# Kernel tuning notes

Hardware: AMD Instinct MI355X
Metric: run time of the kernel (lower is better)

The kernel has to match this reference:

```python
import jax, jax.numpy as jnp
import numpy as np
from jax import lax

V, E, H, K = 100000, 256, 512, 12
B, T = 64, 256
START, END, PAD = 10, 11, 0
NEG = -100000.0


def setup_inputs() -> dict:
    key = jax.random.key(0)
    ks = jax.random.split(key, 16)
    Hd = H // 2
    def n(k, shape, s=0.1):
        return jax.random.normal(k, shape, jnp.float32) * s
    sentence = jax.random.randint(ks[0], (B, T), 0, V)
    sentence_chars = jnp.zeros((B, T, 16), jnp.int32)
    emb = jax.random.normal(ks[1], (V, E), jnp.float32)
    Wih_f, Whh_f = n(ks[2], (4 * Hd, E)), n(ks[3], (4 * Hd, Hd))
    bih_f, bhh_f = n(ks[4], (4 * Hd,)), n(ks[5], (4 * Hd,))
    Wih_b, Whh_b = n(ks[6], (4 * Hd, E)), n(ks[7], (4 * Hd, Hd))
    bih_b, bhh_b = n(ks[8], (4 * Hd,)), n(ks[9], (4 * Hd,))
    Wp, bp = n(ks[10], (K, H)), n(ks[11], (K,))
    # transitions[i, j] = score of transitioning from tag j to tag i
    trans = jax.random.normal(ks[12], (K, K), jnp.float32)
    trans = trans.at[START, :].set(NEG)
    trans = trans.at[:, END].set(NEG)
    trans = trans.at[:, PAD].set(NEG)
    trans = trans.at[PAD, :].set(NEG)
    trans = trans.at[PAD, PAD].set(0.0)
    trans = trans.at[PAD, END].set(0.0)
    h0 = jax.random.normal(ks[13], (2, B, Hd), jnp.float32)
    c0 = jax.random.normal(ks[14], (2, B, Hd), jnp.float32)
    return dict(sentence=sentence, sentence_chars=sentence_chars, emb=emb,
                Wih_f=Wih_f, Whh_f=Whh_f, bih_f=bih_f, bhh_f=bhh_f,
                Wih_b=Wih_b, Whh_b=Whh_b, bih_b=bih_b, bhh_b=bhh_b,
                Wp=Wp, bp=bp, transitions=trans, h0=h0, c0=c0)


def _lstm_dir(x, Wih, Whh, bih, bhh, h, c, reverse):
    # x: [B, T, E] -> hs: [B, T, Hd]; PyTorch LSTM gate order i,f,g,o
    def step(carry, xt):
        h, c = carry
        g = xt @ Wih.T + bih + h @ Whh.T + bhh
        i, f, gg, o = jnp.split(g, 4, axis=-1)
        c = jax.nn.sigmoid(f) * c + jax.nn.sigmoid(i) * jnp.tanh(gg)
        h = jax.nn.sigmoid(o) * jnp.tanh(c)
        return (h, c), h
    _, hs = lax.scan(step, (h, c), jnp.swapaxes(x, 0, 1), reverse=reverse)
    return jnp.swapaxes(hs, 0, 1)


def _viterbi(features, transitions, lengths):
    b, t, k = features.shape
    score0 = jnp.full((b, k), -10000.0, features.dtype).at[:, START].set(0.0)
    def step(score, feat_t):
        m = score[:, None, :] + transitions[None]  # [B, K(to), K(from)]
        bptr = jnp.argmax(m, axis=-1)              # [B, K]
        new = jnp.max(m, axis=-1) + feat_t
        return new, bptr
    final, bptrs = lax.scan(step, score0, jnp.swapaxes(features, 0, 1))  # bptrs [T,B,K]
    best_score = jnp.max(final, axis=-1)
    best_tag = jnp.argmax(final, axis=-1)
    ts = jnp.arange(t)
    def backtrack(x, inp):
        tt, bp = inp  # bp: [B, K]
        emit = x      # p_t (valid where tt < length)
        nxt = jnp.take_along_axis(bp, x[:, None], axis=1)[:, 0]
        x = jnp.where(tt < lengths, nxt, x)
        return x, emit
    _, ps = lax.scan(backtrack, best_tag, (ts, bptrs), reverse=True)  # [T, B]
    paths = jnp.swapaxes(ps, 0, 1)
    paths = jnp.where(jnp.arange(t)[None, :] < lengths[:, None], paths, -1)
    return paths, best_score


def reference(sentence, sentence_chars, emb, Wih_f, Whh_f, bih_f, bhh_f,
              Wih_b, Whh_b, bih_b, bhh_b, Wp, bp, transitions, h0, c0):
    mask = sentence > 0
    lengths = mask.sum(axis=1)
    x = emb[sentence]  # [B, T, E]
    hf = _lstm_dir(x, Wih_f, Whh_f, bih_f, bhh_f, h0[0], c0[0], False)
    hb = _lstm_dir(x, Wih_b, Whh_b, bih_b, bhh_b, h0[1], c0[1], True)
    feats = jnp.concatenate([hf, hb], axis=-1) @ Wp.T + bp  # [B, T, K]
    paths, best_score = _viterbi(feats, transitions, lengths)
    return paths, best_score
```

## Files before the change

### kernel.cpp

```cpp
#include <hip/hip_runtime.h>


#define NB 64
#define NT 256
#define NKTAG 12
#define START_TAG 10
#define KK_SLAB 32
#define KK_REG 16
#define KK_STRM 8

typedef unsigned short u16;
typedef _Float16 half2v __attribute__((ext_vector_type(2)));
typedef _Float16 half8 __attribute__((ext_vector_type(8)));
typedef float f32x4 __attribute__((ext_vector_type(4)));

__device__ __forceinline__ float b2f(u16 u) {
  union { unsigned int i; float f; } v; v.i = ((unsigned int)u) << 16; return v.f;
}
__device__ __forceinline__ u16 f2b(float f) {
  union { float f; unsigned int i; } v; v.f = f;
  unsigned int r = v.i + 0x7FFFu + ((v.i >> 16) & 1u);
  return (u16)(r >> 16);
}
__device__ __forceinline__ u16 f2h(float f) {
  union { _Float16 h; u16 u; } v; v.h = (_Float16)f; return v.u;
}
__device__ __forceinline__ unsigned int pkh(float x, float y) {
  return (unsigned int)f2h(x) | ((unsigned int)f2h(y) << 16);
}
__device__ __forceinline__ float fsig(float x) { return 1.0f / (1.0f + __expf(-x)); }
__device__ __forceinline__ float ftanh(float x) { return 2.0f / (1.0f + __expf(-2.0f * x)) - 1.0f; }

__device__ __forceinline__ float dot2h(unsigned int a, unsigned int b, float c) {
#if __has_builtin(__builtin_amdgcn_fdot2)
  union { unsigned int u; half2v h; } va, vb;
  va.u = a; vb.u = b;
  return __builtin_amdgcn_fdot2(va.h, vb.h, c, false);
#else
  float d;
  asm("v_dot2_f32_f16 %0, %1, %2, %3" : "=v"(d) : "v"(a), "v"(b), "v"(c));
  return d;
#endif
}

__global__ __launch_bounds__(256) void pack_whh(const float* __restrict__ Whf,
                                                const float* __restrict__ Whb,
                                                const float* __restrict__ Wp,
                                                uint4* __restrict__ WT,
                                                unsigned int* __restrict__ WpH) {
  if (blockIdx.x == 256) {
    for (int it = 0; it < 12; ++it) {
      int idx = it * 256 + threadIdx.x;
      int k = idx >> 8, cc = idx & 255;
      WpH[idx] = pkh(Wp[(size_t)k * 512 + 2 * cc], Wp[(size_t)k * 512 + 2 * cc + 1]);
    }
    return;
  }
  int gid = blockIdx.x * 256 + threadIdx.x;
  int d = gid >> 15;
  int rem = gid & 32767;
  int kk = rem >> 8, j = rem & 255;
  const float* W = d ? Whb : Whf;
  int k0 = kk * 2;
  uint4 o;
  o.x = pkh(W[(size_t)j * 256 + k0],         W[(size_t)j * 256 + k0 + 1]);
  o.y = pkh(W[(size_t)(j + 256) * 256 + k0], W[(size_t)(j + 256) * 256 + k0 + 1]);
  o.z = pkh(W[(size_t)(j + 512) * 256 + k0], W[(size_t)(j + 512) * 256 + k0 + 1]);
  o.w = pkh(W[(size_t)(j + 768) * 256 + k0], W[(size_t)(j + 768) * 256 + k0 + 1]);
  WT[gid] = o;
}

__global__ __launch_bounds__(256) void gemm_x(const int* __restrict__ sent,
                                              const float* __restrict__ emb,
                                              const float* __restrict__ Wf,
                                              const float* __restrict__ Wb,
                                              const float* __restrict__ bihf,
                                              const float* __restrict__ bhhf,
                                              const float* __restrict__ bihb,
                                              const float* __restrict__ bhhb,
                                              u16* __restrict__ X4) {
  __shared__ _Float16 A_lds[128][40];
  __shared__ _Float16 B_lds[64][40];
  __shared__ int tok[128];
  __shared__ u16 Xs[128][80];
  int tid = threadIdx.x;
  int in = blockIdx.x;
  int im = blockIdx.y;
  int d = in >> 4, j0 = (in & 15) * 16;
  if (tid < 128) tok[tid] = sent[im * 128 + tid];

  int w = tid >> 6, l = tid & 63;
  int lrow = l & 15, lk = l >> 4;
  f32x4 acc[2][4];
#pragma unroll
  for (int mt = 0; mt < 2; ++mt)
#pragma unroll
    for (int nt = 0; nt < 4; ++nt) acc[mt][nt] = (f32x4)0.0f;

  int arow = tid >> 1, akh = tid & 1;
  int brow = tid & 63, bkq = tid >> 6;
  int r_w = ((brow >> 4) << 8) + j0 + (brow & 15);
  const float* wrow = (d ? Wb : Wf) + (size_t)r_w * 256;

  for (int kc = 0; kc < 8; ++kc) {
    int k0 = kc * 32;
    __syncthreads();
    {
      const float* ap = emb + (size_t)tok[arow] * 256 + k0 + akh * 16;
#pragma unroll
      for (int q = 0; q < 2; ++q) {
        float4 v0 = *(const float4*)(ap + q * 8);
        float4 v1 = *(const float4*)(ap + q * 8 + 4);
        uint4 pk;
        pk.x = pkh(v0.x, v0.y); pk.y = pkh(v0.z, v0.w);
        pk.z = pkh(v1.x, v1.y); pk.w = pkh(v1.z, v1.w);
        *(uint4*)&A_lds[arow][akh * 16 + q * 8] = pk;
      }
    }
    {
      float4 v0 = *(const float4*)(wrow + k0 + bkq * 8);
      float4 v1 = *(const float4*)(wrow + k0 + bkq * 8 + 4);
      uint4 pk;
      pk.x = pkh(v0.x, v0.y); pk.y = pkh(v0.z, v0.w);
      pk.z = pkh(v1.x, v1.y); pk.w = pkh(v1.z, v1.w);
      *(uint4*)&B_lds[brow][bkq * 8] = pk;
    }
    __syncthreads();
    half8 af[2], bf[4];
#pragma unroll
    for (int mt = 0; mt < 2; ++mt)
      af[mt] = *(const half8*)&A_lds[w * 32 + mt * 16 + lrow][lk * 8];
#pragma unroll
    for (int nt = 0; nt < 4; ++nt)
      bf[nt] = *(const half8*)&B_lds[nt * 16 + lrow][lk * 8];
#pragma unroll
    for (int mt = 0; mt < 2; ++mt)
#pragma unroll
      for (int nt = 0; nt < 4; ++nt)
        acc[mt][nt] = __builtin_amdgcn_mfma_f32_16x16x32_f16(af[mt], bf[nt], acc[mt][nt], 0, 0, 0);
  }
  float bias[4];
#pragma unroll
  for (int nt = 0; nt < 4; ++nt) {
    int rr = nt * 256 + j0 + lrow;
    bias[nt] = d ? (bihb[rr] + bhhb[rr]) : (bihf[rr] + bhhf[rr]);
  }
  __syncthreads();
#pragma unroll
  for (int mt = 0; mt < 2; ++mt)
#pragma unroll
    for (int r = 0; r < 4; ++r) {
      int row = w * 32 + mt * 16 + lk * 4 + r;
      uint2 pk;
      pk.x = (unsigned int)f2b(acc[mt][0][r] + bias[0]) |
             ((unsigned int)f2b(acc[mt][1][r] + bias[1]) << 16);
      pk.y = (unsigned int)f2b(acc[mt][2][r] + bias[2]) |
             ((unsigned int)f2b(acc[mt][3][r] + bias[3]) << 16);
      *(uint2*)&Xs[row][lrow * 4] = pk;
    }
  __syncthreads();
  int frow = tid >> 1, fh = tid & 1;
  int i = im * 128 + frow;
  int bb = i >> 8, tt = i & 255;
  size_t base = (((size_t)d * NT + tt) * NB + bb) * 1024 + (size_t)j0 * 4 + fh * 32;
#pragma unroll
  for (int q = 0; q < 4; ++q)
    *(uint4*)&X4[base + q * 8] = *(const uint4*)&Xs[frow][fh * 32 + q * 8];
}

__global__ __launch_bounds__(1024, 4) void lstm_scan(const uint4* __restrict__ WT,
                                                     const ushort4* __restrict__ X4,
                                                     const float* __restrict__ h0,
                                                     const float* __restrict__ c0,
                                                     u16* __restrict__ H) {
  int d = blockIdx.x >> 6, b = blockIdx.x & 63;
  int tid = threadIdx.x;
  int jj = tid & 255, g = tid >> 8;
  __shared__ uint4 wlds[KK_SLAB * 256];
  __shared__ uint4 h2s4[32];
  __shared__ float4 plds[3][256];
  const uint4* Ws = WT + (size_t)d * 32768;
  for (int e = tid; e < KK_SLAB * 256; e += 1024) wlds[e] = Ws[e];
  uint4 wreg[KK_REG];
#pragma unroll
  for (int r = 0; r < KK_REG; ++r)
    wreg[r] = Ws[(size_t)(KK_SLAB + g * KK_REG + r) * 256 + jj];
  float c = 0.f;
  if (g == 0) c = c0[((size_t)d * NB + b) * 256 + jj];
  if (tid < 256) ((u16*)h2s4)[tid] = f2h(h0[((size_t)d * NB + b) * 256 + tid]);
  __syncthreads();
  for (int s = 0; s < NT; ++s) {
    int t = d ? (NT - 1 - s) : s;
    ushort4 xg = make_ushort4(0, 0, 0, 0);
    if (g == 0) xg = X4[(((size_t)d * NT + t) * NB + b) * 256 + jj];
    float ai = 0.f, af = 0.f, ag = 0.f, ao = 0.f;
    {
      uint4 hc0 = h2s4[24 + g * 2], hc1 = h2s4[24 + g * 2 + 1];
      unsigned int hp[8] = {hc0.x, hc0.y, hc0.z, hc0.w, hc1.x, hc1.y, hc1.z, hc1.w};
      const uint4* Wp_ = Ws + (size_t)(96 + g * 8) * 256 + jj;
#pragma unroll
      for (int u = 0; u < KK_STRM; ++u) {
        uint4 wv = Wp_[(size_t)u * 256];
        ai = dot2h(wv.x, hp[u], ai); af = dot2h(wv.y, hp[u], af);
        ag = dot2h(wv.z, hp[u], ag); ao = dot2h(wv.w, hp[u], ao);
      }
    }
    {
      uint4 ha0 = h2s4[g * 2], ha1 = h2s4[g * 2 + 1];
      unsigned int hp[8] = {ha0.x, ha0.y, ha0.z, ha0.w, ha1.x, ha1.y, ha1.z, ha1.w};
#pragma unroll
      for (int r = 0; r < 8; ++r) {
        uint4 wv = wlds[((g * 8 + r) << 8) | jj];
        ai = dot2h(wv.x, hp[r], ai); af = dot2h(wv.y, hp[r], af);
        ag = dot2h(wv.z, hp[r], ag); ao = dot2h(wv.w, hp[r], ao);
      }
    }
    {
      uint4 hb0 = h2s4[8 + g * 4], hb1 = h2s4[8 + g * 4 + 1];
      uint4 hb2 = h2s4[8 + g * 4 + 2], hb3 = h2s4[8 + g * 4 + 3];
      unsigned int hp[16] = {hb0.x, hb0.y, hb0.z, hb0.w, hb1.x, hb1.y, hb1.z, hb1.w,
                             hb2.x, hb2.y, hb2.z, hb2.w, hb3.x, hb3.y, hb3.z, hb3.w};
#pragma unroll
      for (int r = 0; r < KK_REG; ++r) {
        uint4 wv = wreg[r];
        ai = dot2h(wv.x, hp[r], ai); af = dot2h(wv.y, hp[r], af);
        ag = dot2h(wv.z, hp[r], ag); ao = dot2h(wv.w, hp[r], ao);
      }
    }
    if (g) plds[g - 1][jj] = make_float4(ai, af, ag, ao);
    __syncthreads();
    if (g == 0) {
      float4 p0 = plds[0][jj], p1 = plds[1][jj], p2 = plds[2][jj];
      ai += p0.x + p1.x + p2.x + b2f(xg.x);
      af += p0.y + p1.y + p2.y + b2f(xg.y);
      ag += p0.z + p1.z + p2.z + b2f(xg.z);
      ao += p0.w + p1.w + p2.w + b2f(xg.w);
      float ii = fsig(ai), ff = fsig(af), gg = ftanh(ag), oo = fsig(ao);
      c = ff * c + ii * gg;
      float h = oo * ftanh(c);
      u16 hu = f2h(h);
      ((u16*)h2s4)[jj] = hu;
      H[(((size_t)d * NB + b) * NT + t) * 256 + jj] = hu;
    }
    __syncthreads();
  }
}

__global__ __launch_bounds__(384) void feats_kernel(const u16* __restrict__ H,
                                                    const unsigned int* __restrict__ WpH,
                                                    const float* __restrict__ bp,
                                                    float* __restrict__ FT) {
  __shared__ uint4 hbuf[32][65];
  __shared__ uint4 wbuf[64][12];
  int tid = threadIdx.x;
  int i0 = blockIdx.x * 32;
  for (int idx = tid; idx < 768; idx += 384) {
    int it = idx / 12, k = idx - it * 12;
    wbuf[it][k] = ((const uint4*)WpH)[k * 64 + it];
  }
  for (int idx = tid; idx < 2048; idx += 384) {
    int row = idx >> 6, c4 = idx & 63;
    int i = i0 + row;
    int b = i >> 8, t = i & 255;
    int dd = c4 >> 5, cc = c4 & 31;
    const uint4* hp = (const uint4*)(H + (((size_t)dd * NB + b) * NT + t) * 256);
    hbuf[row][c4] = hp[cc];
  }
  __syncthreads();
  int row = tid / 12, k = tid - row * 12;
  float s = 0.f;
#pragma unroll 8
  for (int it = 0; it < 64; ++it) {
    uint4 h4 = hbuf[row][it];
    uint4 w4 = wbuf[it][k];
    s = dot2h(h4.x, w4.x, s); s = dot2h(h4.y, w4.y, s);
    s = dot2h(h4.z, w4.z, s); s = dot2h(h4.w, w4.w, s);
  }
  int i = i0 + row;
  FT[(size_t)i * NKTAG + k] = s + bp[k];
}

__global__ __launch_bounds__(64) void viterbi_kernel(const float* __restrict__ FT,
                                                     const float* __restrict__ trans,
                                                     const int* __restrict__ sent,
                                                     float* __restrict__ out) {
  int b = blockIdx.x, tid = threadIdx.x;
  __shared__ float trans_s[12][12];
  __shared__ float s_s[12];
  __shared__ unsigned char bp_s[256][12];
  __shared__ int path_s[256];
  for (int idx = tid; idx < 144; idx += 64) trans_s[idx / 12][idx % 12] = trans[idx];
  int cnt = 0;
#pragma unroll
  for (int q = 0; q < 4; ++q) cnt += (sent[b * NT + q * 64 + tid] > 0) ? 1 : 0;
  for (int off = 32; off; off >>= 1) cnt += __shfl_down(cnt, off);
  int len = __shfl(cnt, 0);
  if (tid < 12) s_s[tid] = (tid == START_TAG) ? 0.f : -10000.f;
  __syncthreads();
  for (int t = 0; t < NT; ++t) {
    float best = 0.f, f = 0.f;
    int barg = 0;
    if (tid < 12) {
      f = FT[((size_t)b * NT + t) * NKTAG + tid];
      best = s_s[0] + trans_s[tid][0];
      barg = 0;
#pragma unroll
      for (int fr = 1; fr < 12; ++fr) {
        float v = s_s[fr] + trans_s[tid][fr];
        if (v > best) { best = v; barg = fr; }
      }
    }
    __syncthreads();
    if (tid < 12) {
      s_s[tid] = best + f;
      bp_s[t][tid] = (unsigned char)barg;
    }
    __syncthreads();
  }
  if (tid == 0) {
    float bs = s_s[0];
    int bt = 0;
    for (int k = 1; k < 12; ++k)
      if (s_s[k] > bs) { bs = s_s[k]; bt = k; }
    out[NB * NT + b] = bs;
    int x = bt;
    for (int tt = NT - 1; tt >= 0; --tt) {
      path_s[tt] = x;
      int nxt = bp_s[tt][x];
      if (tt < len) x = nxt;
    }
  }
  __syncthreads();
#pragma unroll
  for (int q = 0; q < 4; ++q) {
    int t = q * 64 + tid;
    out[b * NT + t] = (t < len) ? (float)path_s[t] : -1.0f;
  }
}

extern "C" void kernel_launch(void* const* d_in, const int* in_sizes, int n_in,
                              void* d_out, int out_size, void* d_ws, size_t ws_size,
                              hipStream_t stream) {
  (void)in_sizes; (void)n_in; (void)out_size; (void)ws_size;
  const int*   sent  = (const int*)d_in[0];
  const float* emb   = (const float*)d_in[2];
  const float* Wih_f = (const float*)d_in[3];
  const float* Whh_f = (const float*)d_in[4];
  const float* bih_f = (const float*)d_in[5];
  const float* bhh_f = (const float*)d_in[6];
  const float* Wih_b = (const float*)d_in[7];
  const float* Whh_b = (const float*)d_in[8];
  const float* bih_b = (const float*)d_in[9];
  const float* bhh_b = (const float*)d_in[10];
  const float* Wp    = (const float*)d_in[11];
  const float* bp    = (const float*)d_in[12];
  const float* trans = (const float*)d_in[13];
  const float* h0    = (const float*)d_in[14];
  const float* c0    = (const float*)d_in[15];
  float* out = (float*)d_out;

  char* w = (char*)d_ws;
  u16*   X4  = (u16*)w;
  uint4* WTH = (uint4*)(w + 67108864);
  float* FT  = (float*)(w + 67108864 + 1048576);
  unsigned int* WpH = (unsigned int*)(w + 68943872);
  u16*   H   = (u16*)(w + 68956160);

  pack_whh<<<dim3(257), dim3(256), 0, stream>>>(Whh_f, Whh_b, Wp, WTH, WpH);
  gemm_x<<<dim3(32, 128), dim3(256), 0, stream>>>(sent, emb, Wih_f, Wih_b,
                                                  bih_f, bhh_f, bih_b, bhh_b, X4);
  lstm_scan<<<dim3(128), dim3(1024), 0, stream>>>(WTH, (const ushort4*)X4, h0, c0, H);
  feats_kernel<<<dim3(512), dim3(384), 0, stream>>>(H, WpH, bp, FT);
  viterbi_kernel<<<dim3(64), dim3(64), 0, stream>>>(FT, trans, sent, out);
}
```

Before: 599.4 us.

## Split each LSTM sequence across two cooperating blocks with flag-synced hidden exchange

The recurrent scan now runs 256 blocks of 512 threads, with each pair of blocks owning half of the hidden units for one (direction, batch) sequence. The partner blocks swap their fp16 hidden halves every timestep through a global slot buffer and spin on per-block step flags. Each thread's recurrent weights now sit entirely in LDS plus 22 registers, so the per-step global streaming of part of Whh goes away. The cost is a cross-block global handshake every timestep, which adds latency, and the scheme needs both blocks of a pair to be co-resident or it can deadlock.

Result: slower. 1.305 ms (+117.8%).

```diff
diff --git a/kernel.cpp b/kernel.cpp
--- a/kernel.cpp
+++ b/kernel.cpp
@@ -5,9 +5,6 @@
 #define NT 256
 #define NKTAG 12
 #define START_TAG 10
-#define KK_SLAB 32
-#define KK_REG 16
-#define KK_STRM 8
 
 typedef unsigned short u16;
 typedef _Float16 half2v __attribute__((ext_vector_type(2)));
@@ -168,64 +165,74 @@
     *(uint4*)&X4[base + q * 8] = *(const uint4*)&Xs[frow][fh * 32 + q * 8];
 }
 
-__global__ __launch_bounds__(1024, 4) void lstm_scan(const uint4* __restrict__ WT,
-                                                     const ushort4* __restrict__ X4,
-                                                     const float* __restrict__ h0,
-                                                     const float* __restrict__ c0,
-                                                     u16* __restrict__ H) {
-  int d = blockIdx.x >> 6, b = blockIdx.x & 63;
+__global__ __launch_bounds__(512, 2) void lstm_scan(const uint4* __restrict__ WT,
+                                                    const ushort4* __restrict__ X4,
+                                                    const float* __restrict__ h0,
+                                                    const float* __restrict__ c0,
+                                                    u16* __restrict__ H,
+                                                    unsigned int* __restrict__ slotb,
+                                                    int* __restrict__ flags) {
+  int bid = blockIdx.x;
+  int d = bid >> 7, b = (bid >> 1) & 63, p = bid & 1;
+  int pbid = bid ^ 1;
   int tid = threadIdx.x;
-  int jj = tid & 255, g = tid >> 8;
-  __shared__ uint4 wlds[KK_SLAB * 256];
+  int jj = tid & 127, g = tid >> 7;
+  int jbase = p << 7;
+  __shared__ uint4 wlds[5120];
   __shared__ uint4 h2s4[32];
-  __shared__ float4 plds[3][256];
+  __shared__ float4 plds[3][128];
   const uint4* Ws = WT + (size_t)d * 32768;
-  for (int e = tid; e < KK_SLAB * 256; e += 1024) wlds[e] = Ws[e];
-  uint4 wreg[KK_REG];
-#pragma unroll
-  for (int r = 0; r < KK_REG; ++r)
-    wreg[r] = Ws[(size_t)(KK_SLAB + g * KK_REG + r) * 256 + jj];
+#pragma unroll
+  for (int r = 0; r < 10; ++r)
+    wlds[((g * 10 + r) << 7) | jj] = Ws[(size_t)(g * 32 + r) * 256 + jbase + jj];
+  uint4 wreg[22];
+#pragma unroll
+  for (int r = 0; r < 22; ++r)
+    wreg[r] = Ws[(size_t)(g * 32 + 10 + r) * 256 + jbase + jj];
   float c = 0.f;
-  if (g == 0) c = c0[((size_t)d * NB + b) * 256 + jj];
+  if (g == 0) c = c0[((size_t)d * NB + b) * 256 + jbase + jj];
   if (tid < 256) ((u16*)h2s4)[tid] = f2h(h0[((size_t)d * NB + b) * 256 + tid]);
   __syncthreads();
   for (int s = 0; s < NT; ++s) {
     int t = d ? (NT - 1 - s) : s;
     ushort4 xg = make_ushort4(0, 0, 0, 0);
-    if (g == 0) xg = X4[(((size_t)d * NT + t) * NB + b) * 256 + jj];
+    if (g == 0) xg = X4[(((size_t)d * NT + t) * NB + b) * 256 + jbase + jj];
+    if (s > 0 && tid < 16) {
+      if (tid == 0) {
+        while (__hip_atomic_load(&flags[pbid], __ATOMIC_RELAXED,
+                                 __HIP_MEMORY_SCOPE_AGENT) < s - 1) {}
+      }
+      asm volatile("" ::: "memory");
+      unsigned pb = (unsigned)(pbid * 2 + ((s - 1) & 1)) * 64 + tid * 4;
+      uint4 hv;
+      hv.x = __hip_atomic_load(&slotb[pb + 0], __ATOMIC_RELAXED, __HIP_MEMORY_SCOPE_AGENT);
+      hv.y = __hip_atomic_load(&slotb[pb + 1], __ATOMIC_RELAXED, __HIP_MEMORY_SCOPE_AGENT);
+      hv.z = __hip_atomic_load(&slotb[pb + 2], __ATOMIC_RELAXED, __HIP_MEMORY_SCOPE_AGENT);
+      hv.w = __hip_atomic_load(&slotb[pb + 3], __ATOMIC_RELAXED, __HIP_MEMORY_SCOPE_AGENT);
+      h2s4[((1 - p) << 4) + tid] = hv;
+    }
+    __syncthreads();
     float ai = 0.f, af = 0.f, ag = 0.f, ao = 0.f;
-    {
-      uint4 hc0 = h2s4[24 + g * 2], hc1 = h2s4[24 + g * 2 + 1];
-      unsigned int hp[8] = {hc0.x, hc0.y, hc0.z, hc0.w, hc1.x, hc1.y, hc1.z, hc1.w};
-      const uint4* Wp_ = Ws + (size_t)(96 + g * 8) * 256 + jj;
-#pragma unroll
-      for (int u = 0; u < KK_STRM; ++u) {
-        uint4 wv = Wp_[(size_t)u * 256];
-        ai = dot2h(wv.x, hp[u], ai); af = dot2h(wv.y, hp[u], af);
-        ag = dot2h(wv.z, hp[u], ag); ao = dot2h(wv.w, hp[u], ao);
-      }
-    }
-    {
-      uint4 ha0 = h2s4[g * 2], ha1 = h2s4[g * 2 + 1];
-      unsigned int hp[8] = {ha0.x, ha0.y, ha0.z, ha0.w, ha1.x, ha1.y, ha1.z, ha1.w};
-#pragma unroll
-      for (int r = 0; r < 8; ++r) {
-        uint4 wv = wlds[((g * 8 + r) << 8) | jj];
-        ai = dot2h(wv.x, hp[r], ai); af = dot2h(wv.y, hp[r], af);
-        ag = dot2h(wv.z, hp[r], ag); ao = dot2h(wv.w, hp[r], ao);
-      }
-    }
-    {
-      uint4 hb0 = h2s4[8 + g * 4], hb1 = h2s4[8 + g * 4 + 1];
-      uint4 hb2 = h2s4[8 + g * 4 + 2], hb3 = h2s4[8 + g * 4 + 3];
-      unsigned int hp[16] = {hb0.x, hb0.y, hb0.z, hb0.w, hb1.x, hb1.y, hb1.z, hb1.w,
-                             hb2.x, hb2.y, hb2.z, hb2.w, hb3.x, hb3.y, hb3.z, hb3.w};
-#pragma unroll
-      for (int r = 0; r < KK_REG; ++r) {
-        uint4 wv = wreg[r];
-        ai = dot2h(wv.x, hp[r], ai); af = dot2h(wv.y, hp[r], af);
-        ag = dot2h(wv.z, hp[r], ag); ao = dot2h(wv.w, hp[r], ao);
-      }
+    uint4 hv[8];
+#pragma unroll
+    for (int q = 0; q < 8; ++q) hv[q] = h2s4[(g << 3) + q];
+    unsigned int hp[32];
+#pragma unroll
+    for (int q = 0; q < 8; ++q) {
+      hp[q * 4 + 0] = hv[q].x; hp[q * 4 + 1] = hv[q].y;
+      hp[q * 4 + 2] = hv[q].z; hp[q * 4 + 3] = hv[q].w;
+    }
+#pragma unroll
+    for (int r = 0; r < 10; ++r) {
+      uint4 wv = wlds[((g * 10 + r) << 7) | jj];
+      ai = dot2h(wv.x, hp[r], ai); af = dot2h(wv.y, hp[r], af);
+      ag = dot2h(wv.z, hp[r], ag); ao = dot2h(wv.w, hp[r], ao);
+    }
+#pragma unroll
+    for (int r = 0; r < 22; ++r) {
+      uint4 wv = wreg[r];
+      ai = dot2h(wv.x, hp[10 + r], ai); af = dot2h(wv.y, hp[10 + r], af);
+      ag = dot2h(wv.z, hp[10 + r], ag); ao = dot2h(wv.w, hp[10 + r], ao);
     }
     if (g) plds[g - 1][jj] = make_float4(ai, af, ag, ao);
     __syncthreads();
@@ -239,10 +246,20 @@
       c = ff * c + ii * gg;
       float h = oo * ftanh(c);
       u16 hu = f2h(h);
-      ((u16*)h2s4)[jj] = hu;
-      H[(((size_t)d * NB + b) * NT + t) * 256 + jj] = hu;
-    }
-    __syncthreads();
+      ((u16*)h2s4)[jbase + jj] = hu;
+      H[(((size_t)d * NB + b) * NT + t) * 256 + jbase + jj] = hu;
+    }
+    __syncthreads();
+    if (tid < 16) {
+      uint4 ho = h2s4[(p << 4) + tid];
+      unsigned ob = (unsigned)(bid * 2 + (s & 1)) * 64 + tid * 4;
+      __hip_atomic_store(&slotb[ob + 0], ho.x, __ATOMIC_RELAXED, __HIP_MEMORY_SCOPE_AGENT);
+      __hip_atomic_store(&slotb[ob + 1], ho.y, __ATOMIC_RELAXED, __HIP_MEMORY_SCOPE_AGENT);
+      __hip_atomic_store(&slotb[ob + 2], ho.z, __ATOMIC_RELAXED, __HIP_MEMORY_SCOPE_AGENT);
+      __hip_atomic_store(&slotb[ob + 3], ho.w, __ATOMIC_RELAXED, __HIP_MEMORY_SCOPE_AGENT);
+    }
+    if (tid == 0)
+      __hip_atomic_store(&flags[bid], s, __ATOMIC_RELEASE, __HIP_MEMORY_SCOPE_AGENT);
   }
 }
 
@@ -263,8 +280,8 @@
     int i = i0 + row;
     int b = i >> 8, t = i & 255;
     int dd = c4 >> 5, cc = c4 & 31;
-    const uint4* hp = (const uint4*)(H + (((size_t)dd * NB + b) * NT + t) * 256);
-    hbuf[row][c4] = hp[cc];
+    const uint4* hpg = (const uint4*)(H + (((size_t)dd * NB + b) * NT + t) * 256);
+    hbuf[row][c4] = hpg[cc];
   }
   __syncthreads();
   int row = tid / 12, k = tid - row * 12;
@@ -362,14 +379,18 @@
   char* w = (char*)d_ws;
   u16*   X4  = (u16*)w;
   uint4* WTH = (uint4*)(w + 67108864);
-  float* FT  = (float*)(w + 67108864 + 1048576);
+  float* FT  = (float*)(w + 68157440);
   unsigned int* WpH = (unsigned int*)(w + 68943872);
   u16*   H   = (u16*)(w + 68956160);
-
+  unsigned int* slotb = (unsigned int*)(w + 85733376);
+  int*   flags = (int*)(w + 85864448);
+
+  hipMemsetAsync(flags, 0xFF, 1024, stream);
   pack_whh<<<dim3(257), dim3(256), 0, stream>>>(Whh_f, Whh_b, Wp, WTH, WpH);
   gemm_x<<<dim3(32, 128), dim3(256), 0, stream>>>(sent, emb, Wih_f, Wih_b,
                                                   bih_f, bhh_f, bih_b, bhh_b, X4);
-  lstm_scan<<<dim3(128), dim3(1024), 0, stream>>>(WTH, (const ushort4*)X4, h0, c0, H);
+  lstm_scan<<<dim3(256), dim3(512), 0, stream>>>(WTH, (const ushort4*)X4, h0, c0,
+                                                 H, slotb, flags);
   feats_kernel<<<dim3(512), dim3(384), 0, stream>>>(H, WpH, bp, FT);
   viterbi_kernel<<<dim3(64), dim3(64), 0, stream>>>(FT, trans, sent, out);
 }
```

## Store LDS-slab and streamed LSTM recurrent weights as FP8

Applied to the files above, without the earlier changes.

The recurrent weights that the LSTM scan keeps in LDS and those it streams from global memory each step are now packed as FP8 by an extra pack block. In the scan they are unpacked to fp32 and combined with an fp32 copy of h kept in shared memory. This halves LDS footprint and the streamed bytes per step, aiming to cut memory traffic on the sequential critical path. In exchange it adds conversion and scalar FMA work in place of packed dot2 instructions, and FP8 weights lose accuracy, which could flip Viterbi paths.

After: 1.847 ms. 208% more time.

```diff
diff --git a/kernel.cpp b/kernel.cpp
--- a/kernel.cpp
+++ b/kernel.cpp
@@ -9,10 +9,20 @@
 #define KK_REG 16
 #define KK_STRM 8
 
+#if defined(__has_builtin)
+#if __has_builtin(__builtin_amdgcn_cvt_pk_f32_fp8) && __has_builtin(__builtin_amdgcn_cvt_pk_fp8_f32)
+#define HAS_FP8 1
+#endif
+#endif
+#ifndef HAS_FP8
+#define HAS_FP8 0
+#endif
+
 typedef unsigned short u16;
 typedef _Float16 half2v __attribute__((ext_vector_type(2)));
 typedef _Float16 half8 __attribute__((ext_vector_type(8)));
 typedef float f32x4 __attribute__((ext_vector_type(4)));
+typedef float f32x2 __attribute__((ext_vector_type(2)));
 
 __device__ __forceinline__ float b2f(u16 u) {
   union { unsigned int i; float f; } v; v.i = ((unsigned int)u) << 16; return v.f;
@@ -47,13 +57,39 @@
                                                 const float* __restrict__ Whb,
                                                 const float* __restrict__ Wp,
                                                 uint4* __restrict__ WT,
-                                                unsigned int* __restrict__ WpH) {
+                                                unsigned int* __restrict__ WpH,
+                                                uint2* __restrict__ WT8) {
   if (blockIdx.x == 256) {
     for (int it = 0; it < 12; ++it) {
       int idx = it * 256 + threadIdx.x;
       int k = idx >> 8, cc = idx & 255;
       WpH[idx] = pkh(Wp[(size_t)k * 512 + 2 * cc], Wp[(size_t)k * 512 + 2 * cc + 1]);
     }
+    return;
+  }
+  if (blockIdx.x == 257) {
+#if HAS_FP8
+    for (int it = 0; it < 128; ++it) {
+      int idx = it * 256 + threadIdx.x;
+      int d = idx >> 14;
+      int rem = idx & 16383;
+      int q = rem >> 8, j = rem & 255;
+      int kk = (q < 32) ? q : (q + 64);
+      const float* W = d ? Whb : Whf;
+      int k0 = kk * 2;
+      int d0 = 0, d1 = 0;
+      d0 = __builtin_amdgcn_cvt_pk_fp8_f32(W[(size_t)j * 256 + k0],
+                                           W[(size_t)(j + 256) * 256 + k0], d0, false);
+      d0 = __builtin_amdgcn_cvt_pk_fp8_f32(W[(size_t)(j + 512) * 256 + k0],
+                                           W[(size_t)(j + 768) * 256 + k0], d0, true);
+      d1 = __builtin_amdgcn_cvt_pk_fp8_f32(W[(size_t)j * 256 + k0 + 1],
+                                           W[(size_t)(j + 256) * 256 + k0 + 1], d1, false);
+      d1 = __builtin_amdgcn_cvt_pk_fp8_f32(W[(size_t)(j + 512) * 256 + k0 + 1],
+                                           W[(size_t)(j + 768) * 256 + k0 + 1], d1, true);
+      uint2 o; o.x = (unsigned int)d0; o.y = (unsigned int)d1;
+      WT8[idx] = o;
+    }
+#endif
     return;
   }
   int gid = blockIdx.x * 256 + threadIdx.x;
@@ -169,6 +205,7 @@
 }
 
 __global__ __launch_bounds__(1024, 4) void lstm_scan(const uint4* __restrict__ WT,
+                                                     const uint2* __restrict__ WT8,
                                                      const ushort4* __restrict__ X4,
                                                      const float* __restrict__ h0,
                                                      const float* __restrict__ c0,
@@ -176,24 +213,81 @@
   int d = blockIdx.x >> 6, b = blockIdx.x & 63;
   int tid = threadIdx.x;
   int jj = tid & 255, g = tid >> 8;
-  __shared__ uint4 wlds[KK_SLAB * 256];
   __shared__ uint4 h2s4[32];
   __shared__ float4 plds[3][256];
+#if HAS_FP8
+  __shared__ uint2 wlds8[KK_SLAB * 256];
+  __shared__ float hf32[256];
+  const uint2* W8 = WT8 + (size_t)d * 16384;
+  for (int e = tid; e < KK_SLAB * 256; e += 1024) wlds8[e] = W8[e];
+#else
+  __shared__ uint4 wlds[KK_SLAB * 256];
+#endif
   const uint4* Ws = WT + (size_t)d * 32768;
+#if !HAS_FP8
   for (int e = tid; e < KK_SLAB * 256; e += 1024) wlds[e] = Ws[e];
+#endif
   uint4 wreg[KK_REG];
 #pragma unroll
   for (int r = 0; r < KK_REG; ++r)
     wreg[r] = Ws[(size_t)(KK_SLAB + g * KK_REG + r) * 256 + jj];
   float c = 0.f;
   if (g == 0) c = c0[((size_t)d * NB + b) * 256 + jj];
-  if (tid < 256) ((u16*)h2s4)[tid] = f2h(h0[((size_t)d * NB + b) * 256 + tid]);
+  if (tid < 256) {
+    float hv = h0[((size_t)d * NB + b) * 256 + tid];
+    ((u16*)h2s4)[tid] = f2h(hv);
+#if HAS_FP8
+    hf32[tid] = hv;
+#endif
+  }
   __syncthreads();
   for (int s = 0; s < NT; ++s) {
     int t = d ? (NT - 1 - s) : s;
     ushort4 xg = make_ushort4(0, 0, 0, 0);
     if (g == 0) xg = X4[(((size_t)d * NT + t) * NB + b) * 256 + jj];
     float ai = 0.f, af = 0.f, ag = 0.f, ao = 0.f;
+#if HAS_FP8
+    const float4* hf4 = (const float4*)hf32;
+    {
+      float4 a0 = hf4[48 + g * 4], a1 = hf4[48 + g * 4 + 1];
+      float4 a2 = hf4[48 + g * 4 + 2], a3 = hf4[48 + g * 4 + 3];
+      float hv[8 * 2] = {a0.x, a0.y, a0.z, a0.w, a1.x, a1.y, a1.z, a1.w,
+                         a2.x, a2.y, a2.z, a2.w, a3.x, a3.y, a3.z, a3.w};
+      const uint2* Wst = W8 + (size_t)(32 + g * 8) * 256 + jj;
+#pragma unroll
+      for (int u = 0; u < KK_STRM; ++u) {
+        uint2 wv = Wst[(size_t)u * 256];
+        f32x2 pif0 = __builtin_amdgcn_cvt_pk_f32_fp8(wv.x, false);
+        f32x2 pgo0 = __builtin_amdgcn_cvt_pk_f32_fp8(wv.x, true);
+        f32x2 pif1 = __builtin_amdgcn_cvt_pk_f32_fp8(wv.y, false);
+        f32x2 pgo1 = __builtin_amdgcn_cvt_pk_f32_fp8(wv.y, true);
+        float hA = hv[2 * u], hB = hv[2 * u + 1];
+        ai += pif0.x * hA + pif1.x * hB;
+        af += pif0.y * hA + pif1.y * hB;
+        ag += pgo0.x * hA + pgo1.x * hB;
+        ao += pgo0.y * hA + pgo1.y * hB;
+      }
+    }
+    {
+      float4 a0 = hf4[g * 4], a1 = hf4[g * 4 + 1];
+      float4 a2 = hf4[g * 4 + 2], a3 = hf4[g * 4 + 3];
+      float hv[8 * 2] = {a0.x, a0.y, a0.z, a0.w, a1.x, a1.y, a1.z, a1.w,
+                         a2.x, a2.y, a2.z, a2.w, a3.x, a3.y, a3.z, a3.w};
+#pragma unroll
+      for (int r = 0; r < 8; ++r) {
+        uint2 wv = wlds8[((g * 8 + r) << 8) | jj];
+        f32x2 pif0 = __builtin_amdgcn_cvt_pk_f32_fp8(wv.x, false);
+        f32x2 pgo0 = __builtin_amdgcn_cvt_pk_f32_fp8(wv.x, true);
+        f32x2 pif1 = __builtin_amdgcn_cvt_pk_f32_fp8(wv.y, false);
+        f32x2 pgo1 = __builtin_amdgcn_cvt_pk_f32_fp8(wv.y, true);
+        float hA = hv[2 * r], hB = hv[2 * r + 1];
+        ai += pif0.x * hA + pif1.x * hB;
+        af += pif0.y * hA + pif1.y * hB;
+        ag += pgo0.x * hA + pgo1.x * hB;
+        ao += pgo0.y * hA + pgo1.y * hB;
+      }
+    }
+#else
     {
       uint4 hc0 = h2s4[24 + g * 2], hc1 = h2s4[24 + g * 2 + 1];
       unsigned int hp[8] = {hc0.x, hc0.y, hc0.z, hc0.w, hc1.x, hc1.y, hc1.z, hc1.w};
@@ -215,6 +309,7 @@
         ag = dot2h(wv.z, hp[r], ag); ao = dot2h(wv.w, hp[r], ao);
       }
     }
+#endif
     {
       uint4 hb0 = h2s4[8 + g * 4], hb1 = h2s4[8 + g * 4 + 1];
       uint4 hb2 = h2s4[8 + g * 4 + 2], hb3 = h2s4[8 + g * 4 + 3];
@@ -240,6 +335,9 @@
       float h = oo * ftanh(c);
       u16 hu = f2h(h);
       ((u16*)h2s4)[jj] = hu;
+#if HAS_FP8
+      hf32[jj] = h;
+#endif
       H[(((size_t)d * NB + b) * NT + t) * 256 + jj] = hu;
     }
     __syncthreads();
@@ -263,8 +361,8 @@
     int i = i0 + row;
     int b = i >> 8, t = i & 255;
     int dd = c4 >> 5, cc = c4 & 31;
-    const uint4* hp = (const uint4*)(H + (((size_t)dd * NB + b) * NT + t) * 256);
-    hbuf[row][c4] = hp[cc];
+    const uint4* hpg = (const uint4*)(H + (((size_t)dd * NB + b) * NT + t) * 256);
+    hbuf[row][c4] = hpg[cc];
   }
   __syncthreads();
   int row = tid / 12, k = tid - row * 12;
@@ -362,14 +460,16 @@
   char* w = (char*)d_ws;
   u16*   X4  = (u16*)w;
   uint4* WTH = (uint4*)(w + 67108864);
-  float* FT  = (float*)(w + 67108864 + 1048576);
+  float* FT  = (float*)(w + 68157440);
   unsigned int* WpH = (unsigned int*)(w + 68943872);
   u16*   H   = (u16*)(w + 68956160);
-
-  pack_whh<<<dim3(257), dim3(256), 0, stream>>>(Whh_f, Whh_b, Wp, WTH, WpH);
+  uint2* WT8 = (uint2*)(w + 85733376);
+
+  pack_whh<<<dim3(258), dim3(256), 0, stream>>>(Whh_f, Whh_b, Wp, WTH, WpH, WT8);
   gemm_x<<<dim3(32, 128), dim3(256), 0, stream>>>(sent, emb, Wih_f, Wih_b,
                                                   bih_f, bhh_f, bih_b, bhh_b, X4);
-  lstm_scan<<<dim3(128), dim3(1024), 0, stream>>>(WTH, (const ushort4*)X4, h0, c0, H);
+  lstm_scan<<<dim3(128), dim3(1024), 0, stream>>>(WTH, WT8, (const ushort4*)X4,
+                                                  h0, c0, H);
   feats_kernel<<<dim3(512), dim3(384), 0, stream>>>(H, WpH, bp, FT);
   viterbi_kernel<<<dim3(64), dim3(64), 0, stream>>>(FT, trans, sent, out);
 }
```
